# Optimization experiments

Hardware: AMD Instinct MI355X
Metric: run time of the kernel (lower is better)

The kernel has to match this reference:

```python
import jax, jax.numpy as jnp
import numpy as np

P = 4          # num_perturbations
N = 50000      # nodes
E = 800000     # edges
IN = 64        # input_dim == hidden_dim (allows stacked conv weights)
H = 64         # args.hidden_dim
OUT = 10       # output_dim (classes)
G = 512        # num graphs in batch
DROP_P = 0.1   # node-drop prob p
EPS = 1e-5     # BatchNorm eps


def setup_inputs() -> dict:
    key = jax.random.key(0)
    ks = jax.random.split(key, 8)
    x = jax.random.normal(ks[0], (N, IN), jnp.float32)
    edge_index = jax.random.randint(ks[1], (2, E), 0, N, dtype=jnp.int64)
    batch = jnp.sort(jax.random.randint(ks[2], (N,), 0, G, dtype=jnp.int64))
    drop_mask = jax.random.bernoulli(ks[3], DROP_P, (P, N))
    conv_w = jax.random.normal(ks[4], (4, H, H), jnp.float32) * (1.0 / np.sqrt(H))
    conv_b = jnp.zeros((4, H), jnp.float32)
    bn_gamma = jnp.ones((4, H), jnp.float32)
    bn_beta = jnp.zeros((4, H), jnp.float32)
    fc_w = jax.random.normal(ks[5], (5, H, OUT), jnp.float32) * (1.0 / np.sqrt(H))
    fc_b = jnp.zeros((5, OUT), jnp.float32)
    return {"x": x, "edge_index": edge_index, "batch": batch, "drop_mask": drop_mask,
            "conv_w": conv_w, "conv_b": conv_b, "bn_gamma": bn_gamma,
            "bn_beta": bn_beta, "fc_w": fc_w, "fc_b": fc_b}


def reference(x, edge_index, batch, drop_mask, conv_w, conv_b, bn_gamma, bn_beta, fc_w, fc_b):
    P_, N_ = drop_mask.shape
    n_tot = P_ * N_
    # node dropping per perturbation: x -> [P, N, F] with dropped rows zeroed
    x_rep = jnp.where(drop_mask[:, :, None], jnp.zeros((), x.dtype), x[None, :, :])
    # replicate edge_index across perturbations with offset (max+1), as in torch code
    offset = jnp.max(edge_index) + 1
    shift = offset * jnp.arange(P_, dtype=edge_index.dtype)[:, None]
    src = (edge_index[0][None, :] + shift).reshape(-1)
    dst = (edge_index[1][None, :] + shift).reshape(-1)
    # GCN symmetric normalization with self-loops (PyG GCNConv default)
    deg = jax.ops.segment_sum(jnp.ones(src.shape, jnp.float32), dst, num_segments=n_tot) + 1.0
    dinv = jax.lax.rsqrt(deg)
    norm_e = dinv[src] * dinv[dst]        # edge messages
    norm_s = dinv * dinv                   # self-loop messages

    h = x_rep.reshape(n_tot, -1)
    outs = [x_rep]
    for i in range(4):
        hw = h @ conv_w[i]                 # [n_tot, H]
        agg = jax.ops.segment_sum(norm_e[:, None] * hw[src], dst, num_segments=n_tot)
        h = agg + norm_s[:, None] * hw + conv_b[i]
        # BatchNorm1d (training mode: batch stats, biased variance)
        mu = h.mean(axis=0)
        var = h.var(axis=0)
        h = (h - mu) * jax.lax.rsqrt(var + EPS) * bn_gamma[i] + bn_beta[i]
        h = jax.nn.relu(h)
        outs.append(h.reshape(P_, N_, -1))

    out = None
    for i, o in enumerate(outs):
        pooled = jax.ops.segment_sum(o.mean(axis=0), batch, num_segments=G)  # global_add_pool
        y = pooled @ fc_w[i] + fc_b[i]     # dropout skipped (eval)
        out = y if out is None else out + y
    return jax.nn.log_softmax(out, axis=-1)
```

## Files before the change

kernel.cpp:

```cpp
#include <hip/hip_runtime.h>

#define N_NODES 50000
#define N_EDGES 800000
#define P_PERT  4
#define NTOT    (P_PERT * N_NODES)
#define HDIM    64
#define NGRAPH  512
#define NCLASS  10
#define BN_EPS  1e-5f
#define SCAN_BLOCKS ((N_NODES + 255) / 256)
#define BN_SLICES 64
#define SAH_STRIDE 72
#define SC_STRIDE 72
#define ZERO_FLOATS 297120
#define PSTRIDE ((size_t)(N_NODES + 1) * 32)
#define GATHER_BLOCKS (((N_NODES + 63) / 64) * 8)

typedef _Float16 half4 __attribute__((ext_vector_type(4)));
typedef _Float16 f16x8 __attribute__((ext_vector_type(8)));
typedef float    f32x4 __attribute__((ext_vector_type(4)));
typedef unsigned short u16x8 __attribute__((ext_vector_type(8)));



__global__ void count_kernel(const int* __restrict__ ei, int* __restrict__ cnt) {
    int j = blockIdx.x * blockDim.x + threadIdx.x;
    if (j >= N_EDGES) return;
    atomicAdd(&cnt[ei[N_EDGES + j]], 1);
}

__global__ void scan_reduce(const int* __restrict__ cnt, int* __restrict__ bsum,
                            float* __restrict__ dinv) {
    __shared__ int sdata[256];
    int i = blockIdx.x * 256 + threadIdx.x;
    int v = (i < N_NODES) ? cnt[i] : 0;
    if (i < N_NODES) dinv[i] = rsqrtf((float)v + 1.0f);
    sdata[threadIdx.x] = (v + 7) & ~7;
    __syncthreads();
    for (int off = 128; off > 0; off >>= 1) {
        if (threadIdx.x < off) sdata[threadIdx.x] += sdata[threadIdx.x + off];
        __syncthreads();
    }
    if (threadIdx.x == 0) bsum[blockIdx.x] = sdata[0];
}

__global__ void scan_tops(const int* __restrict__ bsum, int* __restrict__ boff,
                          int* __restrict__ rowptr) {
    __shared__ int sdata[256];
    int t = threadIdx.x;
    int v = (t < SCAN_BLOCKS) ? bsum[t] : 0;
    sdata[t] = v;
    __syncthreads();
    for (int off = 1; off < 256; off <<= 1) {
        int tmp = (t >= off) ? sdata[t - off] : 0;
        __syncthreads();
        sdata[t] += tmp;
        __syncthreads();
    }
    if (t < SCAN_BLOCKS) boff[t] = sdata[t] - v;
    if (t == 255) rowptr[N_NODES] = sdata[255];
}

__global__ void scan_write(const int* __restrict__ cnt, const int* __restrict__ boff,
                           int* __restrict__ rowptr) {
    __shared__ int sdata[256];
    int i = blockIdx.x * 256 + threadIdx.x;
    int v = (i < N_NODES) ? ((cnt[i] + 7) & ~7) : 0;
    sdata[threadIdx.x] = v;
    __syncthreads();
    for (int off = 1; off < 256; off <<= 1) {
        int tmp = (threadIdx.x >= off) ? sdata[threadIdx.x - off] : 0;
        __syncthreads();
        sdata[threadIdx.x] += tmp;
        __syncthreads();
    }
    if (i < N_NODES) rowptr[i] = boff[blockIdx.x] + sdata[threadIdx.x] - v;
}

__global__ void fill_kernel(const int* __restrict__ ei, const int* __restrict__ rowptr,
                            int* __restrict__ cursor, unsigned short* __restrict__ csr) {
    int j = blockIdx.x * blockDim.x + threadIdx.x;
    if (j >= N_EDGES) return;
    int s = ei[j], d = ei[N_EDGES + j];
    int pos = rowptr[d] + atomicAdd(&cursor[d], 1);
    csr[pos] = (unsigned short)s;
}

__global__ void pad_kernel(const int* __restrict__ cnt, const int* __restrict__ rowptr,
                           unsigned short* __restrict__ csr) {
    int v = blockIdx.x * 256 + threadIdx.x;
    if (v >= N_NODES) return;
    int c = cnt[v], cp = (c + 7) & ~7, base = rowptr[v];
    for (int j = c; j < cp; ++j) csr[base + j] = (unsigned short)N_NODES;
}

__global__ void wpack_zero_kernel(const float* __restrict__ W, _Float16* __restrict__ wpack,
                                  float* __restrict__ zreg, _Float16* __restrict__ hwh2) {
    int idx = blockIdx.x * 256 + threadIdx.x;
    if (idx < 4 * 4096) {
        int e = idx & 4095;
        int j = e & 7;
        int lane = (e >> 3) & 63;
        int ntkh = e >> 9;
        int kh = ntkh >> 2, nt = ntkh & 3;
        int m = lane & 15, quad = lane >> 4;
        wpack[idx] = (_Float16)W[(idx >> 12) * 4096 + (kh * 32 + quad * 8 + j) * 64 + nt * 16 + m];
    }
    if (idx < 256) {
        hwh2[(size_t)(idx >> 5) * PSTRIDE + (size_t)N_NODES * 32 + (idx & 31)] = (_Float16)0.0f;
    }
    for (int i = idx; i < ZERO_FLOATS; i += gridDim.x * 256) zreg[i] = 0.0f;
}

__global__ void bn_reduce(const float* __restrict__ bn, const float* __restrict__ gamma,
                          const float* __restrict__ beta, float* __restrict__ bnss) {
    int f = threadIdx.x;
    if (f >= 64) return;
    float su = 0.0f, sq = 0.0f;
    for (int s = 0; s < BN_SLICES; ++s) {
        su += bn[s * 128 + f];
        sq += bn[s * 128 + 64 + f];
    }
    const float inv_n = 1.0f / (float)NTOT;
    float mu = su * inv_n;
    float var = sq * inv_n - mu * mu;
    float sc = gamma[f] * rsqrtf(var + BN_EPS);
    bnss[f] = sc;
    bnss[64 + f] = beta[f] - mu * sc;
}

template <int LAYER0>
__global__ __launch_bounds__(256) void gemm_fused(const void* __restrict__ srcv,
        const int* __restrict__ mask, const float* __restrict__ bnss,
        const int* __restrict__ batch, const _Float16* __restrict__ wpack,
        const float* __restrict__ dinv, _Float16* __restrict__ hwh,
        float* __restrict__ pooled) {
    __shared__ _Float16 sAh[64 * SAH_STRIDE];
    __shared__ _Float16 sC[64 * SC_STRIDE];
    int tid = threadIdx.x;
    size_t rowbase = (size_t)blockIdx.x * 64;
    int lane = tid & 63;
    int wv = tid >> 6;
    int bg[16];
#pragma unroll
    for (int rr = 0; rr < 16; ++rr)
        bg[rr] = batch[(int)((rowbase + wv * 16 + rr) % N_NODES)];
    const f16x8* wp = (const f16x8*)wpack;
    f16x8 bfrag[2][4];
#pragma unroll
    for (int kh = 0; kh < 2; ++kh)
#pragma unroll
        for (int nt = 0; nt < 4; ++nt)
            bfrag[kh][nt] = wp[(kh * 4 + nt) * 64 + lane];
    int r0 = tid >> 4;
    int f4l = (tid & 15) * 4;
    float4 sc4, sh4;
    if (!LAYER0) {
        sc4 = *(const float4*)&bnss[f4l];
        sh4 = *(const float4*)&bnss[64 + f4l];
    }
#pragma unroll
    for (int it = 0; it < 4; ++it) {
        int r = r0 + it * 16;
        int grow = (int)rowbase + r;
        float4 val;
        if (LAYER0) {
            const float* src = (const float*)srcv;
            int p = grow / N_NODES, v = grow - p * N_NODES;
            if (mask[p * N_NODES + v]) {
                val = make_float4(0.f, 0.f, 0.f, 0.f);
            } else {
                val = *(const float4*)&src[(size_t)v * HDIM + f4l];
            }
        } else {
            const _Float16* src = (const _Float16*)srcv;
            half4 hv = *(const half4*)&src[(size_t)grow * HDIM + f4l];
            val.x = fmaxf((float)hv.x * sc4.x + sh4.x, 0.0f);
            val.y = fmaxf((float)hv.y * sc4.y + sh4.y, 0.0f);
            val.z = fmaxf((float)hv.z * sc4.z + sh4.z, 0.0f);
            val.w = fmaxf((float)hv.w * sc4.w + sh4.w, 0.0f);
        }
        half4 hv4 = {(_Float16)val.x, (_Float16)val.y, (_Float16)val.z, (_Float16)val.w};
        *(half4*)&sAh[r * SAH_STRIDE + f4l] = hv4;
    }
    __syncthreads();
    int m = lane & 15;
    int quad = lane >> 4;
    f32x4 acc4[4];
#pragma unroll
    for (int nt = 0; nt < 4; ++nt) acc4[nt] = (f32x4){0.f, 0.f, 0.f, 0.f};
#pragma unroll
    for (int kh = 0; kh < 2; ++kh) {
        f16x8 a = *(const f16x8*)&sAh[(wv * 16 + m) * SAH_STRIDE + kh * 32 + quad * 8];
#pragma unroll
        for (int nt = 0; nt < 4; ++nt)
            acc4[nt] = __builtin_amdgcn_mfma_f32_16x16x32_f16(a, bfrag[kh][nt], acc4[nt], 0, 0, 0);
    }
#pragma unroll
    for (int reg = 0; reg < 4; ++reg) {
        int crow = wv * 16 + quad * 4 + reg;
        int growc = (int)rowbase + crow;
        int vc = growc % N_NODES;
        float dsc = dinv[vc];
#pragma unroll
        for (int nt = 0; nt < 4; ++nt)
            sC[crow * SC_STRIDE + nt * 16 + m] = (_Float16)(acc4[nt][reg] * dsc);
    }
    __syncthreads();
    {
        int r = tid >> 2, c = tid & 3;
        int grow = (int)rowbase + r;
        int p = grow / N_NODES, v = grow - p * N_NODES;
        _Float16* dst0 = &hwh[(size_t)(p * 2 + 0) * PSTRIDE + (size_t)v * 32];
        _Float16* dst1 = &hwh[(size_t)(p * 2 + 1) * PSTRIDE + (size_t)v * 32];
        *(f16x8*)&dst0[c * 8] = *(f16x8*)&sC[r * SC_STRIDE + c * 8];
        *(f16x8*)&dst1[c * 8] = *(f16x8*)&sC[r * SC_STRIDE + (c + 4) * 8];
    }
    {
        int f = lane;
        int curg = -1;
        float acc = 0.0f;
#pragma unroll
        for (int rr = 0; rr < 16; ++rr) {
            int g = bg[rr];
            if (g != curg) {
                if (curg >= 0) atomicAdd(&pooled[curg * HDIM + f], acc * (1.0f / P_PERT));
                curg = g;
                acc = 0.0f;
            }
            acc += (float)sAh[(wv * 16 + rr) * SAH_STRIDE + f];
        }
        atomicAdd(&pooled[curg * HDIM + f], acc * (1.0f / P_PERT));
    }
}

__global__ __launch_bounds__(256) void gather_bn(const _Float16* __restrict__ hwh2,
        const int* __restrict__ rowptr, const unsigned short* __restrict__ csr,
        const float* __restrict__ dinv, const float* __restrict__ b,
        _Float16* __restrict__ h, float* __restrict__ bn) {
    __shared__ float lsum[4][4][8];
    __shared__ float lssq[4][4][8];
    int tid = threadIdx.x;
    int lane = tid & 63;
    int wv = tid >> 6;
    int part = blockIdx.x & 7;
    int grp = blockIdx.x >> 3;
    int p = part >> 1, fh = part & 1;
    int n16 = lane >> 2;
    int f16 = lane & 3;
    int v = grp * 64 + wv * 16 + n16;
    bool valid = v < N_NODES;
    int vv = valid ? v : N_NODES;
    int kb = 0, ke = 0;
    float di = 0.0f;
    if (valid) { kb = rowptr[v]; ke = rowptr[v + 1]; di = dinv[v]; }
    const _Float16* lsrc = hwh2 + (size_t)part * PSTRIDE + f16 * 8;
    f16x8 sv = *(const f16x8*)&lsrc[(size_t)vv * 32];
    float acc[8];
#pragma unroll
    for (int j = 0; j < 8; ++j) acc[j] = 0.0f;
    u16x8 ci = {};
    if (kb < ke) ci = *(const u16x8*)&csr[kb];
    for (int k = kb; k < ke; k += 8) {
        u16x8 cin = {};
        if (k + 8 < ke) cin = *(const u16x8*)&csr[k + 8];
        f16x8 m0 = *(const f16x8*)&lsrc[(size_t)ci[0] * 32];
        f16x8 m1 = *(const f16x8*)&lsrc[(size_t)ci[1] * 32];
        f16x8 m2 = *(const f16x8*)&lsrc[(size_t)ci[2] * 32];
        f16x8 m3 = *(const f16x8*)&lsrc[(size_t)ci[3] * 32];
        f16x8 m4 = *(const f16x8*)&lsrc[(size_t)ci[4] * 32];
        f16x8 m5 = *(const f16x8*)&lsrc[(size_t)ci[5] * 32];
        f16x8 m6 = *(const f16x8*)&lsrc[(size_t)ci[6] * 32];
        f16x8 m7 = *(const f16x8*)&lsrc[(size_t)ci[7] * 32];
        f16x8 s = ((m0 + m1) + (m2 + m3)) + ((m4 + m5) + (m6 + m7));
#pragma unroll
        for (int j = 0; j < 8; ++j) acc[j] += (float)s[j];
        ci = cin;
    }
    float hv[8], qv[8];
    float4 b0 = *(const float4*)&b[fh * 32 + f16 * 8];
    float4 b1 = *(const float4*)&b[fh * 32 + f16 * 8 + 4];
    float bb[8] = {b0.x, b0.y, b0.z, b0.w, b1.x, b1.y, b1.z, b1.w};
#pragma unroll
    for (int j = 0; j < 8; ++j) {
        float x = valid ? fmaf(di, acc[j] + (float)sv[j], bb[j]) : 0.0f;
        hv[j] = x;
        qv[j] = x * x;
    }
    if (valid) {
        f16x8 hh;
#pragma unroll
        for (int j = 0; j < 8; ++j) hh[j] = (_Float16)hv[j];
        __builtin_nontemporal_store(hh,
            (f16x8*)&h[((size_t)p * N_NODES + (size_t)v) * HDIM + fh * 32 + f16 * 8]);
    }
#pragma unroll
    for (int d = 4; d <= 32; d <<= 1) {
#pragma unroll
        for (int j = 0; j < 8; ++j) {
            hv[j] += __shfl_xor(hv[j], d);
            qv[j] += __shfl_xor(qv[j], d);
        }
    }
    if (lane < 4) {
#pragma unroll
        for (int j = 0; j < 8; ++j) {
            lsum[wv][f16][j] = hv[j];
            lssq[wv][f16][j] = qv[j];
        }
    }
    __syncthreads();
    if (tid < 32) {
        int q = tid >> 3, j = tid & 7;
        float s = lsum[0][q][j] + lsum[1][q][j] + lsum[2][q][j] + lsum[3][q][j];
        float qq = lssq[0][q][j] + lssq[1][q][j] + lssq[2][q][j] + lssq[3][q][j];
        float* bns = bn + (blockIdx.x & (BN_SLICES - 1)) * 128;
        int f = fh * 32 + q * 8 + j;
        atomicAdd(&bns[f], s);
        atomicAdd(&bns[64 + f], qq);
    }
}

__global__ void final_pool(const _Float16* __restrict__ h, const float* __restrict__ bnss,
                           const int* __restrict__ batch, float* __restrict__ pooled) {
    int t = blockIdx.x * blockDim.x + threadIdx.x;
    if (t >= N_NODES * HDIM) return;
    int v = t >> 6, f = t & 63;
    float sc = bnss[f], sh = bnss[64 + f];
    float s = 0.0f;
#pragma unroll
    for (int p = 0; p < P_PERT; ++p) {
        size_t idx = ((size_t)(p * N_NODES + v)) * HDIM + f;
        s += fmaxf((float)h[idx] * sc + sh, 0.0f);
    }
    atomicAdd(&pooled[batch[v] * HDIM + f], s * (1.0f / P_PERT));
}

__global__ void head_kernel(const float* __restrict__ pooled, const float* __restrict__ fcw,
                            const float* __restrict__ fcb, float* __restrict__ out) {
    int g = blockIdx.x;
    __shared__ float y[NCLASS];
    __shared__ float lse;
    int c = threadIdx.x;
    if (c < NCLASS) {
        float acc = 0.0f;
        for (int i = 0; i < 5; ++i) {
            acc += fcb[i * NCLASS + c];
            const float* pr = &pooled[((size_t)i * NGRAPH + g) * HDIM];
            const float* w = &fcw[i * HDIM * NCLASS + c];
            for (int k = 0; k < HDIM; ++k) acc += pr[k] * w[k * NCLASS];
        }
        y[c] = acc;
    }
    __syncthreads();
    if (threadIdx.x == 0) {
        float m = y[0];
        for (int i = 1; i < NCLASS; ++i) m = fmaxf(m, y[i]);
        float s = 0.0f;
        for (int i = 0; i < NCLASS; ++i) s += expf(y[i] - m);
        lse = m + logf(s);
    }
    __syncthreads();
    if (c < NCLASS) out[g * NCLASS + c] = y[c] - lse;
}

extern "C" void kernel_launch(void* const* d_in, const int* in_sizes, int n_in,
                              void* d_out, int out_size, void* d_ws, size_t ws_size,
                              hipStream_t stream) {
    const float* x      = (const float*)d_in[0];
    const int*   ei     = (const int*)d_in[1];
    const int*   batch  = (const int*)d_in[2];
    const int*   mask   = (const int*)d_in[3];
    const float* conv_w = (const float*)d_in[4];
    const float* conv_b = (const float*)d_in[5];
    const float* gamma  = (const float*)d_in[6];
    const float* beta   = (const float*)d_in[7];
    const float* fcw    = (const float*)d_in[8];
    const float* fcb    = (const float*)d_in[9];
    float* out = (float*)d_out;

    char* ws = (char*)d_ws;
    int*      cnt     = (int*)(ws + 0);
    int*      cursor  = (int*)(ws + 200000);
    float*    pooled  = (float*)(ws + 400000);
    float*    bn      = (float*)(ws + 1055360);
    float*    bnss    = (float*)(ws + 1186432);
    int*      rowptr  = (int*)(ws + 1188480);
    float*    dinv    = (float*)(ws + 1388484);
    unsigned short* csr = (unsigned short*)(ws + 1588496);
    _Float16* h       = (_Float16*)(ws + 3989504);
    _Float16* hwh     = (_Float16*)(ws + 29589504);
    int*      bsum    = (int*)(ws + 55190016);
    int*      boff    = (int*)(ws + 55191040);
    _Float16* wpack   = (_Float16*)(ws + 55192064);

    wpack_zero_kernel<<<512, 256, 0, stream>>>(conv_w, wpack, (float*)ws, hwh);
    count_kernel<<<(N_EDGES + 255) / 256, 256, 0, stream>>>(ei, cnt);
    scan_reduce<<<SCAN_BLOCKS, 256, 0, stream>>>(cnt, bsum, dinv);
    scan_tops<<<1, 256, 0, stream>>>(bsum, boff, rowptr);
    scan_write<<<SCAN_BLOCKS, 256, 0, stream>>>(cnt, boff, rowptr);
    fill_kernel<<<(N_EDGES + 255) / 256, 256, 0, stream>>>(ei, rowptr, cursor, csr);
    pad_kernel<<<SCAN_BLOCKS, 256, 0, stream>>>(cnt, rowptr, csr);

    for (int i = 0; i < 4; ++i) {
        float* bni = bn + i * BN_SLICES * 128;
        if (i == 0)
            gemm_fused<1><<<NTOT / 64, 256, 0, stream>>>(x, mask, nullptr,
                                                         batch, wpack, dinv, hwh, pooled);
        else
            gemm_fused<0><<<NTOT / 64, 256, 0, stream>>>(h, nullptr, bnss + (i - 1) * 128,
                                                         batch, wpack + (size_t)i * 4096,
                                                         dinv, hwh,
                                                         pooled + (size_t)i * NGRAPH * HDIM);
        gather_bn<<<GATHER_BLOCKS, 256, 0, stream>>>(hwh, rowptr, csr, dinv,
                                                     conv_b + i * HDIM, h, bni);
        bn_reduce<<<1, 64, 0, stream>>>(bni, gamma + i * HDIM, beta + i * HDIM,
                                        bnss + i * 128);
    }
    final_pool<<<(N_NODES * HDIM + 255) / 256, 256, 0, stream>>>(
        h, bnss + 3 * 128, batch, pooled + (size_t)4 * NGRAPH * HDIM);
    head_kernel<<<NGRAPH, 64, 0, stream>>>(pooled, fcw, fcb, out);
}
```

Measured before the change: 441.5 us.

## Reuse count-atomic slots for CSR fill, widen BN reduce, batch pooling atomics

```diff
diff --git a/kernel.cpp b/kernel.cpp
--- a/kernel.cpp
+++ b/kernel.cpp
@@ -23,10 +23,11 @@
 
 
 
-__global__ void count_kernel(const int* __restrict__ ei, int* __restrict__ cnt) {
+__global__ void count_kernel(const int* __restrict__ ei, int* __restrict__ cnt,
+                             int* __restrict__ slot) {
     int j = blockIdx.x * blockDim.x + threadIdx.x;
     if (j >= N_EDGES) return;
-    atomicAdd(&cnt[ei[N_EDGES + j]], 1);
+    slot[j] = atomicAdd(&cnt[ei[N_EDGES + j]], 1);
 }
 
 __global__ void scan_reduce(const int* __restrict__ cnt, int* __restrict__ bsum,
@@ -78,12 +79,11 @@
 }
 
 __global__ void fill_kernel(const int* __restrict__ ei, const int* __restrict__ rowptr,
-                            int* __restrict__ cursor, unsigned short* __restrict__ csr) {
+                            const int* __restrict__ slot, unsigned short* __restrict__ csr) {
     int j = blockIdx.x * blockDim.x + threadIdx.x;
     if (j >= N_EDGES) return;
     int s = ei[j], d = ei[N_EDGES + j];
-    int pos = rowptr[d] + atomicAdd(&cursor[d], 1);
-    csr[pos] = (unsigned short)s;
+    csr[rowptr[d] + slot[j]] = (unsigned short)s;
 }
 
 __global__ void pad_kernel(const int* __restrict__ cnt, const int* __restrict__ rowptr,
@@ -114,19 +114,26 @@
 
 __global__ void bn_reduce(const float* __restrict__ bn, const float* __restrict__ gamma,
                           const float* __restrict__ beta, float* __restrict__ bnss) {
-    int f = threadIdx.x;
-    if (f >= 64) return;
-    float su = 0.0f, sq = 0.0f;
-    for (int s = 0; s < BN_SLICES; ++s) {
-        su += bn[s * 128 + f];
-        sq += bn[s * 128 + 64 + f];
-    }
-    const float inv_n = 1.0f / (float)NTOT;
-    float mu = su * inv_n;
-    float var = sq * inv_n - mu * mu;
-    float sc = gamma[f] * rsqrtf(var + BN_EPS);
-    bnss[f] = sc;
-    bnss[64 + f] = beta[f] - mu * sc;
+    __shared__ float part[4][128];
+    __shared__ float tot[128];
+    int t = threadIdx.x;
+    int f = t & 127, q = t >> 7;
+    float s = 0.0f;
+#pragma unroll
+    for (int i = 0; i < 16; ++i) s += bn[(q * 16 + i) * 128 + f];
+    part[q][f] = s;
+    __syncthreads();
+    if (t < 128) tot[t] = part[0][t] + part[1][t] + part[2][t] + part[3][t];
+    __syncthreads();
+    if (t < 64) {
+        float su = tot[t], sq = tot[64 + t];
+        const float inv_n = 1.0f / (float)NTOT;
+        float mu = su * inv_n;
+        float var = sq * inv_n - mu * mu;
+        float sc = gamma[t] * rsqrtf(var + BN_EPS);
+        bnss[t] = sc;
+        bnss[64 + t] = beta[t] - mu * sc;
+    }
 }
 
 template <int LAYER0>
@@ -323,17 +330,31 @@
 
 __global__ void final_pool(const _Float16* __restrict__ h, const float* __restrict__ bnss,
                            const int* __restrict__ batch, float* __restrict__ pooled) {
-    int t = blockIdx.x * blockDim.x + threadIdx.x;
-    if (t >= N_NODES * HDIM) return;
-    int v = t >> 6, f = t & 63;
+    int f = threadIdx.x & 63;
+    int sg = threadIdx.x >> 6;
+    int vb = blockIdx.x * 16 + sg * 4;
     float sc = bnss[f], sh = bnss[64 + f];
-    float s = 0.0f;
-#pragma unroll
-    for (int p = 0; p < P_PERT; ++p) {
-        size_t idx = ((size_t)(p * N_NODES + v)) * HDIM + f;
-        s += fmaxf((float)h[idx] * sc + sh, 0.0f);
-    }
-    atomicAdd(&pooled[batch[v] * HDIM + f], s * (1.0f / P_PERT));
+    int curg = -1;
+    float acc = 0.0f;
+#pragma unroll
+    for (int i = 0; i < 4; ++i) {
+        int v = vb + i;
+        if (v >= N_NODES) break;
+        float s = 0.0f;
+#pragma unroll
+        for (int p = 0; p < P_PERT; ++p) {
+            size_t idx = ((size_t)(p * N_NODES + v)) * HDIM + f;
+            s += fmaxf((float)h[idx] * sc + sh, 0.0f);
+        }
+        int g = batch[v];
+        if (g != curg) {
+            if (curg >= 0) atomicAdd(&pooled[curg * HDIM + f], acc * (1.0f / P_PERT));
+            curg = g;
+            acc = 0.0f;
+        }
+        acc += s;
+    }
+    if (curg >= 0) atomicAdd(&pooled[curg * HDIM + f], acc * (1.0f / P_PERT));
 }
 
 __global__ void head_kernel(const float* __restrict__ pooled, const float* __restrict__ fcw,
@@ -381,7 +402,6 @@
 
     char* ws = (char*)d_ws;
     int*      cnt     = (int*)(ws + 0);
-    int*      cursor  = (int*)(ws + 200000);
     float*    pooled  = (float*)(ws + 400000);
     float*    bn      = (float*)(ws + 1055360);
     float*    bnss    = (float*)(ws + 1186432);
@@ -393,13 +413,14 @@
     int*      bsum    = (int*)(ws + 55190016);
     int*      boff    = (int*)(ws + 55191040);
     _Float16* wpack   = (_Float16*)(ws + 55192064);
+    int*      slot    = (int*)(ws + 55224832);
 
     wpack_zero_kernel<<<512, 256, 0, stream>>>(conv_w, wpack, (float*)ws, hwh);
-    count_kernel<<<(N_EDGES + 255) / 256, 256, 0, stream>>>(ei, cnt);
+    count_kernel<<<(N_EDGES + 255) / 256, 256, 0, stream>>>(ei, cnt, slot);
     scan_reduce<<<SCAN_BLOCKS, 256, 0, stream>>>(cnt, bsum, dinv);
     scan_tops<<<1, 256, 0, stream>>>(bsum, boff, rowptr);
     scan_write<<<SCAN_BLOCKS, 256, 0, stream>>>(cnt, boff, rowptr);
-    fill_kernel<<<(N_EDGES + 255) / 256, 256, 0, stream>>>(ei, rowptr, cursor, csr);
+    fill_kernel<<<(N_EDGES + 255) / 256, 256, 0, stream>>>(ei, rowptr, slot, csr);
     pad_kernel<<<SCAN_BLOCKS, 256, 0, stream>>>(cnt, rowptr, csr);
 
     for (int i = 0; i < 4; ++i) {
@@ -414,10 +435,10 @@
                                                          pooled + (size_t)i * NGRAPH * HDIM);
         gather_bn<<<GATHER_BLOCKS, 256, 0, stream>>>(hwh, rowptr, csr, dinv,
                                                      conv_b + i * HDIM, h, bni);
-        bn_reduce<<<1, 64, 0, stream>>>(bni, gamma + i * HDIM, beta + i * HDIM,
-                                        bnss + i * 128);
-    }
-    final_pool<<<(N_NODES * HDIM + 255) / 256, 256, 0, stream>>>(
+        bn_reduce<<<1, 512, 0, stream>>>(bni, gamma + i * HDIM, beta + i * HDIM,
+                                         bnss + i * 128);
+    }
+    final_pool<<<(N_NODES + 15) / 16, 256, 0, stream>>>(
         h, bnss + 3 * 128, batch, pooled + (size_t)4 * NGRAPH * HDIM);
     head_kernel<<<NGRAPH, 64, 0, stream>>>(pooled, fcw, fcb, out);
 }
```

New measurement: 399.1 us, median of 2. -9.6%, faster.
